# Optimization experiments

Measured on AMD Instinct MI355X. Metric: run time of the kernel, lower is better.

Reference implementation:

```python
import jax, jax.numpy as jnp
import numpy as np

M = 256      # num memories in bnn_history
D = 7686     # input_size (2 agent one-hot + 7680 embedding + 4 scalars)
H = 256      # NEAT hidden nodes
O = 4        # NEAT output nodes
N = D + H + O  # total nodes in dense weight matrix


def setup_inputs() -> dict:
    key = jax.random.key(0)
    ks = jax.random.split(key, 8)
    inv_sqrt_d = 1.0 / np.sqrt(D).astype(np.float32)
    return {
        "input_matrix": jax.random.normal(ks[0], (M, D), jnp.float32),
        "Wq": jax.random.normal(ks[1], (D, D), jnp.float32) * inv_sqrt_d,
        "bq": jnp.zeros((D,), jnp.float32),
        "Wk": jax.random.normal(ks[2], (D, D), jnp.float32) * inv_sqrt_d,
        "bk": jnp.zeros((D,), jnp.float32),
        "Wv": jax.random.normal(ks[3], (D, D), jnp.float32) * inv_sqrt_d,
        "bv": jnp.zeros((D,), jnp.float32),
        "weight_mu": jax.random.normal(ks[4], (N, N), jnp.float32) * 0.01,
        "weight_sigma": jnp.full((N, N), 0.1, jnp.float32),  # build_network inits sigma to 0.1
        "bias_mu": jnp.zeros((H + O,), jnp.float32),
        "bias_sigma": jnp.full((H + O,), 0.1, jnp.float32),
        "eps_w": jax.random.normal(ks[5], (N, N), jnp.float32),
        "eps_b": jax.random.normal(ks[6], (H + O,), jnp.float32),
    }


def reference(input_matrix, Wq, bq, Wk, bk, Wv, bv,
              weight_mu, weight_sigma, bias_mu, bias_sigma, eps_w, eps_b):
    # --- attention over memory rows (nn.Linear applies x @ W.T + b) ---
    Q = input_matrix @ Wq.T + bq            # [M, D]
    K = input_matrix @ Wk.T + bk            # [M, D]
    V = input_matrix @ Wv.T + bv            # [M, D]
    scale = 1.0 / jnp.sqrt(jnp.asarray(D, input_matrix.dtype))
    attn = jax.nn.softmax((Q @ K.T) * scale, axis=-1)  # [M, M]
    context = (attn @ V).mean(axis=0)       # [D] pooled attended context

    # --- Bayesian reparameterized genome weights / biases ---
    W = weight_mu + weight_sigma * eps_w    # [N, N], W[i, j] = weight of edge i->j
    b = bias_mu + bias_sigma * eps_b        # [H+O]

    # --- topological NEAT-style evaluation: inputs, then hidden, then outputs ---
    values0 = jnp.zeros((N,), input_matrix.dtype).at[:D].set(context)

    def step(values, j):
        col = jax.lax.dynamic_slice_in_dim(W, j, 1, axis=1)[:, 0]  # incoming weights of node j
        pre = values @ col + b[j - D]        # sum aggregation + bias
        return values.at[j].set(jnp.tanh(pre)), None

    values, _ = jax.lax.scan(step, values0, jnp.arange(D, N))
    return values[-O:]                       # output node activations
```

## Files before the change

kernel.cpp:

```cpp
#include <hip/hip_runtime.h>
#include <hip/hip_bf16.h>
#include <type_traits>

#define DIN   7686
#define NNODE 7946
#define HOUT  260
#define KP    8192
#define BROW  1036

typedef __attribute__((ext_vector_type(8))) short bf16x8;
typedef __attribute__((ext_vector_type(4))) float f32x4;
typedef __attribute__((ext_vector_type(2))) float f32x2;

__device__ __forceinline__ unsigned int f2b(float f) {
  union { float f; unsigned int u; } v; v.f = f;
  return (v.u + 0x7FFFu + ((v.u >> 16) & 1u)) >> 16;
}
__device__ __forceinline__ unsigned int pack2(float lo, float hi) {
  unsigned int r;
  asm("v_cvt_pk_bf16_f32 %0, %1, %2" : "=v"(r) : "v"(lo), "v"(hi));
  return r;
}
__device__ __forceinline__ float b2f(unsigned short h) {
  union { unsigned int u; float f; } v; v.u = ((unsigned int)h) << 16; return v.f;
}
__device__ __forceinline__ float readlane_f(float v, int lane) {
  return __uint_as_float(__builtin_amdgcn_readlane(__float_as_uint(v), lane));
}

__global__ void prep_x2(const float* __restrict__ X, char* __restrict__ XbT2)
{
  const int m = blockIdx.x, t = threadIdx.x;
  const float* row = X + (size_t)m * DIN;
  const int i16 = m >> 4;
#pragma unroll
  for (int c2 = 0; c2 < 4; ++c2) {
    const int k8 = (c2 * 256 + t) * 8;
    float f[8];
    if (k8 + 8 <= DIN) {
#pragma unroll
      for (int h = 0; h < 4; ++h) {
        float2 v = *(const float2*)(row + k8 + h * 2);
        f[h * 2] = v.x; f[h * 2 + 1] = v.y;
      }
    } else {
#pragma unroll
      for (int h = 0; h < 8; ++h) f[h] = (k8 + h < DIN) ? row[k8 + h] : 0.f;
    }
    uint4 o;
    o.x = pack2(f[0], f[1]); o.y = pack2(f[2], f[3]);
    o.z = pack2(f[4], f[5]); o.w = pack2(f[6], f[7]);
    const int kc = k8 >> 7, kk = k8 & 127, ks = kk >> 5, hq = (kk & 31) >> 3;
    const int lane = (m & 15) + (hq << 4);
    char* dst = XbT2 + ((((size_t)kc * 16 + i16) * 4 + ks) << 10) + lane * 16;
    *(uint4*)dst = o;
  }
}

__global__ __launch_bounds__(512, 4)
void gemm_qk9(const char* __restrict__ XbT2,
              const float* __restrict__ Wq, const float* __restrict__ Wk,
              const float* __restrict__ bq, const float* __restrict__ bk,
              unsigned short* __restrict__ Qbf, unsigned short* __restrict__ Kbf)
{
  const int nt = blockIdx.x, mat = blockIdx.y;
  const float* W = mat ? Wk : Wq;
  const float* bias = mat ? bk : bq;
  unsigned short* Out = mat ? Kbf : Qbf;
  const int n0 = nt * 32;
  const int tid = threadIdx.x, l = tid & 63, wv = tid >> 6;
  const int lm = l & 15, hq = l >> 4;

  __shared__ __align__(16) unsigned short Bp[32 * BROW];

  const long long DD = (long long)DIN * DIN;

  f32x4 acc[2][2] = {};
  bf16x8 A0[2], A1[2], A2[2];
  f32x4 F[16];

  long long rb[4];
#pragma unroll
  for (int r = 0; r < 4; ++r) {
    int grow = n0 + wv * 4 + r; if (grow > DIN - 1) grow = DIN - 1;
    rb[r] = (long long)grow * DIN;
  }

#define LOADW(z_) {                                                       \
    const int k0_ = (z_) * 1024;                                          \
    _Pragma("unroll")                                                     \
    for (int r_ = 0; r_ < 4; ++r_)                                        \
      _Pragma("unroll")                                                   \
      for (int c_ = 0; c_ < 4; ++c_) {                                    \
        long long gi_ = rb[r_] + k0_ + c_ * 256 + l * 4;                  \
        if (gi_ > DD - 4) gi_ = DD - 4;       \
        F[r_ * 4 + c_] = __builtin_nontemporal_load((const f32x4*)(W + gi_)); \
      } }

#define WRITEW() {                                                        \
    _Pragma("unroll")                                                     \
    for (int r_ = 0; r_ < 4; ++r_) {                                      \
      unsigned short* dr_ = &Bp[(wv * 4 + r_) * BROW];                    \
      _Pragma("unroll")                                                   \
      for (int c_ = 0; c_ < 4; ++c_) {                                    \
        f32x4 v_ = F[r_ * 4 + c_];                                        \
        uint2 o_; o_.x = pack2(v_[0], v_[1]); o_.y = pack2(v_[2], v_[3]); \
        *(uint2*)(dr_ + c_ * 256 + l * 4) = o_;                           \
      } } }

#define LA(dst, z_, s_) {                                                 \
    const int kc_ = (z_) * 8 + ((s_) >> 2), ks_ = (s_) & 3;               \
    const char* b_ = XbT2 +                                               \
        ((((size_t)kc_ * 16 + 2 * wv) * 4 + ks_) << 10) + l * 16;         \
    dst[0] = *(const bf16x8*)b_;                                          \
    dst[1] = *(const bf16x8*)(b_ + 4096); }

#define STEP(Ar, s_) {                                                    \
    bf16x8 b0_ = *(const bf16x8*)&Bp[lm * BROW + (s_) * 32 + hq * 8];     \
    bf16x8 b1_ = *(const bf16x8*)&Bp[(16 + lm) * BROW + (s_) * 32 + hq * 8]; \
    acc[0][0] = __builtin_amdgcn_mfma_f32_16x16x32_bf16(Ar[0], b0_, acc[0][0], 0, 0, 0); \
    acc[0][1] = __builtin_amdgcn_mfma_f32_16x16x32_bf16(Ar[0], b1_, acc[0][1], 0, 0, 0); \
    acc[1][0] = __builtin_amdgcn_mfma_f32_16x16x32_bf16(Ar[1], b0_, acc[1][0], 0, 0, 0); \
    acc[1][1] = __builtin_amdgcn_mfma_f32_16x16x32_bf16(Ar[1], b1_, acc[1][1], 0, 0, 0); }

#pragma unroll 1
  for (int z = 0; z < 8; ++z) {
    if (z) __syncthreads();

    LOADW(z)
    WRITEW()
    __syncthreads();

    LA(A0, z, 0) LA(A1, z, 1) LA(A2, z, 2)
#pragma unroll 1
    for (int su = 0; su < 30; su += 3) {
      STEP(A0, su + 0)
      if (su + 3 < 32) LA(A0, z, su + 3)
      STEP(A1, su + 1)
      if (su + 4 < 32) LA(A1, z, su + 4)
      STEP(A2, su + 2)
      if (su + 5 < 32) LA(A2, z, su + 5)
    }
    STEP(A0, 30)
    STEP(A1, 31)
  }
#undef LOADW
#undef WRITEW
#undef LA
#undef STEP

#pragma unroll
  for (int i = 0; i < 2; ++i) {
    const int r0 = (2 * wv + i) * 16 + hq * 4;
#pragma unroll
    for (int j = 0; j < 2; ++j) {
      const int col = n0 + j * 16 + lm;
      const float bb = (col < DIN) ? bias[col] : 0.f;
#pragma unroll
      for (int q = 0; q < 4; ++q) {
        const float v = acc[i][j][q] + bb;
        Out[(size_t)(r0 + q) * KP + col] = (col < DIN) ? (unsigned short)f2b(v) : 0;
      }
    }
  }
}

__global__ __launch_bounds__(512)
void gemm_logits(const unsigned short* __restrict__ Qbf,
                 const unsigned short* __restrict__ Kbf, float* __restrict__ LP)
{
  const int qr = blockIdx.x & 1, qc = blockIdx.x >> 1, z = blockIdx.z;
  const int tid = threadIdx.x, lane = tid & 63, wv = tid >> 6;
  const int lm = lane & 15, lq = (lane >> 4) * 8;
  const int rowBase = qr * 128 + (wv & 3) * 32;
  const int colBase = qc * 128 + (wv >> 2) * 64;
  const int k0 = z * 512;
  f32x4 acc[2][4] = {};
#pragma unroll 4
  for (int ks = 0; ks < 16; ++ks) {
    bf16x8 a[2], b[4];
#pragma unroll
    for (int i = 0; i < 2; ++i)
      a[i] = *(const bf16x8*)(Qbf + (size_t)(rowBase + i * 16 + lm) * KP + k0 + ks * 32 + lq);
#pragma unroll
    for (int j = 0; j < 4; ++j)
      b[j] = *(const bf16x8*)(Kbf + (size_t)(colBase + j * 16 + lm) * KP + k0 + ks * 32 + lq);
#pragma unroll
    for (int i = 0; i < 2; ++i)
#pragma unroll
      for (int j = 0; j < 4; ++j)
        acc[i][j] = __builtin_amdgcn_mfma_f32_16x16x32_bf16(a[i], b[j], acc[i][j], 0, 0, 0);
  }
  float* out = LP + (size_t)z * 65536;
#pragma unroll
  for (int i = 0; i < 2; ++i) {
    const int r0 = rowBase + i * 16 + (lane >> 4) * 4;
#pragma unroll
    for (int j = 0; j < 4; ++j) {
      const int col = colBase + j * 16 + lm;
#pragma unroll
      for (int q = 0; q < 4; ++q)
        out[(size_t)(r0 + q) * 256 + col] = acc[i][j][q];
    }
  }
}

__global__ void softmax_fused(const float* __restrict__ LP, float* __restrict__ abar)
{
  __shared__ float red[8];
  const int m = blockIdx.x, t = threadIdx.x;
  float v = 0.f;
#pragma unroll
  for (int zz = 0; zz < 16; ++zz) v += LP[(size_t)zz * 65536 + m * 256 + t];
  const float scale = 1.0f / sqrtf((float)DIN);
  float mx = v;
#pragma unroll
  for (int o = 32; o >= 1; o >>= 1) mx = fmaxf(mx, __shfl_xor(mx, o, 64));
  if ((t & 63) == 0) red[t >> 6] = mx;
  __syncthreads();
  mx = fmaxf(fmaxf(red[0], red[1]), fmaxf(red[2], red[3]));
  float e = __expf((v - mx) * scale);
  float s = e;
#pragma unroll
  for (int o = 32; o >= 1; o >>= 1) s += __shfl_xor(s, o, 64);
  if ((t & 63) == 0) red[4 + (t >> 6)] = s;
  __syncthreads();
  s = red[4] + red[5] + red[6] + red[7];
  atomicAdd(&abar[t], e * (1.0f / 256.0f) / s);
}

__global__ void y_kernel(const float* __restrict__ X, const float* __restrict__ abar,
                         float* __restrict__ y)
{
  __shared__ float ab[256];
  ab[threadIdx.x] = abar[threadIdx.x];
  __syncthreads();
  const int c = blockIdx.x * 256 + threadIdx.x;
  if (c >= DIN) return;
  float s = 0.f;
#pragma unroll 8
  for (int m = 0; m < 256; ++m) s += ab[m] * X[(size_t)m * DIN + c];
  y[c] = s;
}

__global__ __launch_bounds__(512)
void ctx_mv(const float* __restrict__ Wv, const float* __restrict__ y,
            const float* __restrict__ bv, float* __restrict__ ctx)
{
  const int wv = threadIdx.x >> 6, l = threadIdx.x & 63;
  const int row = blockIdx.x * 8 + wv;
  if (row >= DIN) return;
  const float* wr_ = Wv + (size_t)row * DIN;
  float s = 0.f;
#pragma unroll 5
  for (int it = 0; it < 30; ++it) {
    const int k = it * 256 + l * 4;
    f32x4 w4 = __builtin_nontemporal_load((const f32x4*)(wr_ + k));
    float4 y4 = *(const float4*)(y + k);
    s = fmaf(w4[0], y4.x, s);
    s = fmaf(w4[1], y4.y, s);
    s = fmaf(w4[2], y4.z, s);
    s = fmaf(w4[3], y4.w, s);
  }
  if (l < 6) s += wr_[7680 + l] * y[7680 + l];
#pragma unroll
  for (int o = 32; o >= 1; o >>= 1) s += __shfl_xor(s, o, 64);
  if (l == 0) ctx[row] = s + bv[row];
}

__global__ void base_kernel(const float* __restrict__ mu, const float* __restrict__ sg,
                            const float* __restrict__ ep, const float* __restrict__ ctx,
                            float* __restrict__ base)
{
  const int j = threadIdx.x;
  if (j >= HOUT) return;
  const int i0 = blockIdx.x * 31;
  const int i1 = min(i0 + 31, DIN);
  float acc = 0.f;
#pragma unroll 4
  for (int i = i0; i < i1; ++i) {
    const size_t idx = (size_t)i * NNODE + DIN + j;
    acc = fmaf(ctx[i], fmaf(sg[idx], ep[idx], mu[idx]), acc);
  }
  atomicAdd(&base[j], acc);
}

__global__ void ws_kernel(const float* __restrict__ mu, const float* __restrict__ sg,
                          const float* __restrict__ ep, float* __restrict__ WsG)
{
  const int t = blockIdx.x;
  const int j = threadIdx.x;
  if (j >= HOUT) return;
  const size_t idx = (size_t)(DIN + t) * NNODE + DIN + j;
  WsG[t * HOUT + j] = fmaf(sg[idx], ep[idx], mu[idx]);
}

__global__ __launch_bounds__(64, 1)
void scan2(const float* __restrict__ WsG, const float* __restrict__ base,
           const float* __restrict__ bmu, const float* __restrict__ bsg,
           const float* __restrict__ epb, float* __restrict__ out)
{
  __shared__ __align__(16) float tile[32 * HOUT + 128];
  const int l = threadIdx.x;

  float a0, a1, a2, a3, a4;
  {
    int j = l;       a0 = base[j] + bmu[j] + bsg[j] * epb[j];
    j = l + 64;      a1 = base[j] + bmu[j] + bsg[j] * epb[j];
    j = l + 128;     a2 = base[j] + bmu[j] + bsg[j] * epb[j];
    j = l + 192;     a3 = base[j] + bmu[j] + bsg[j] * epb[j];
    j = l + 256;     a4 = (j < HOUT) ? (base[j] + bmu[j] + bsg[j] * epb[j]) : 0.f;
  }

  float4 stg[33];
  auto LOADT = [&](int tb) {
    const int nfl = ((tb == 8) ? 4 : 32) * HOUT;
    const float* src = WsG + tb * 32 * HOUT;
#pragma unroll
    for (int c = 0; c < 33; ++c) {
      const int o = c * 256 + l * 4;
      if (o < nfl) stg[c] = *(const float4*)(src + o);
    }
  };
  auto WRITET = [&](int tb) {
    const int nfl = ((tb == 8) ? 4 : 32) * HOUT;
#pragma unroll
    for (int c = 0; c < 33; ++c) {
      const int o = c * 256 + l * 4;
      if (o < nfl) *(float4*)&tile[o] = stg[c];
    }
  };

  float w0, w1, w2, w3, w4;
  auto PRER = [&](int trow) {
    const float* tr = tile + trow * HOUT;
    w0 = tr[l]; w1 = tr[l + 64]; w2 = tr[l + 128]; w3 = tr[l + 192]; w4 = tr[l + 256];
  };

  auto inner = [&](auto Bc, int tb, int nrows) {
    constexpr int B = Bc.value;
    for (int tt = 0; tt < nrows; ++tt) {
      const int t = tb * 32 + tt;
      float pre;
      if constexpr (B == 0) pre = readlane_f(a0, t & 63);
      else if constexpr (B == 1) pre = readlane_f(a1, t & 63);
      else if constexpr (B == 2) pre = readlane_f(a2, t & 63);
      else if constexpr (B == 3) pre = readlane_f(a3, t & 63);
      else pre = readlane_f(a4, t & 63);
      const float pc = fminf(fmaxf(pre, -12.f), 12.f);
      const float e = __expf(2.f * pc);
      const float vt = 1.f - 2.f / (e + 1.f);
      if (t >= 256 && l == 0) out[t - 256] = vt;
      if (l > t)            a0 = fmaf(vt, w0, a0);
      if (l + 64 > t)       a1 = fmaf(vt, w1, a1);
      if (l + 128 > t)      a2 = fmaf(vt, w2, a2);
      if (l + 192 > t)      a3 = fmaf(vt, w3, a3);
      if (l + 256 > t && l + 256 < HOUT) a4 = fmaf(vt, w4, a4);
      if (tt + 1 < nrows) PRER(tt + 1);
    }
  };

  LOADT(0); WRITET(0); PRER(0);

#define TILE_STEP(tb, B, nr)                                    \
  { if ((tb) < 8) LOADT((tb) + 1);                              \
    inner(std::integral_constant<int, B>{}, (tb), (nr));        \
    if ((tb) < 8) { WRITET((tb) + 1); PRER(0); } }

  TILE_STEP(0, 0, 32)
  TILE_STEP(1, 0, 32)
  TILE_STEP(2, 1, 32)
  TILE_STEP(3, 1, 32)
  TILE_STEP(4, 2, 32)
  TILE_STEP(5, 2, 32)
  TILE_STEP(6, 3, 32)
  TILE_STEP(7, 3, 32)
  TILE_STEP(8, 4, 4)
#undef TILE_STEP
}

extern "C" void kernel_launch(void* const* d_in, const int* in_sizes, int n_in,
                              void* d_out, int out_size, void* d_ws, size_t ws_size,
                              hipStream_t stream)
{
  const float* X   = (const float*)d_in[0];
  const float* Wq  = (const float*)d_in[1];
  const float* bq  = (const float*)d_in[2];
  const float* Wk  = (const float*)d_in[3];
  const float* bk  = (const float*)d_in[4];
  const float* Wv  = (const float*)d_in[5];
  const float* bv  = (const float*)d_in[6];
  const float* wmu = (const float*)d_in[7];
  const float* wsg = (const float*)d_in[8];
  const float* bmu = (const float*)d_in[9];
  const float* bsg = (const float*)d_in[10];
  const float* epw = (const float*)d_in[11];
  const float* epb = (const float*)d_in[12];

  char* p = (char*)d_ws;
  auto alloc = [&](size_t bytes) -> char* {
    char* r = p;
    p += (bytes + 255) & ~(size_t)255;
    return r;
  };
  char* XbT2 = alloc((size_t)64 * 65536);
  unsigned short* Qbf = (unsigned short*)alloc((size_t)256 * KP * 2);
  unsigned short* Kbf = (unsigned short*)alloc((size_t)256 * KP * 2);
  float* LP   = (float*)alloc((size_t)16 * 65536 * 4);
  float* abar = (float*)alloc(256 * 4);
  float* y    = (float*)alloc(7686 * 4);
  float* ctx  = (float*)alloc(7686 * 4);
  float* base = (float*)alloc(HOUT * 4);
  float* WsG  = (float*)alloc((size_t)HOUT * HOUT * 4 + 1024);

  prep_x2<<<dim3(256), dim3(256), 0, stream>>>(X, XbT2);
  (void)hipMemsetAsync(abar, 0, 256 * 4, stream);
  (void)hipMemsetAsync(base, 0, HOUT * 4, stream);
  (void)hipMemsetAsync(Qbf, 0, (size_t)256 * KP * 2, stream);
  (void)hipMemsetAsync(Kbf, 0, (size_t)256 * KP * 2, stream);

  gemm_qk9<<<dim3(241, 2), dim3(512), 0, stream>>>(XbT2, Wq, Wk, bq, bk, Qbf, Kbf);
  gemm_logits<<<dim3(4, 1, 16), dim3(512), 0, stream>>>(Qbf, Kbf, LP);
  softmax_fused<<<dim3(256), dim3(256), 0, stream>>>(LP, abar);
  y_kernel<<<dim3(31), dim3(256), 0, stream>>>(X, abar, y);
  ctx_mv<<<dim3(961), dim3(512), 0, stream>>>(Wv, y, bv, ctx);
  base_kernel<<<dim3(256), dim3(320), 0, stream>>>(wmu, wsg, epw, ctx, base);
  ws_kernel<<<dim3(260), dim3(320), 0, stream>>>(wmu, wsg, epw, WsG);
  scan2<<<dim3(1), dim3(64), 0, stream>>>(WsG, base, bmu, bsg, epb, (float*)d_out);
}
```

Before: 350.1 us.

## Widen QK GEMM tile to 64 columns with smaller K chunks; move ws_kernel earlier

The Q/K projection kernel now computes 64 output columns per block instead of 32, with K staged in chunks of 512 instead of 1024. The chunk is loaded in two register halves to cap register use. Each A fragment loaded from global memory now feeds 8 MFMAs instead of 4, halving the re-reads of the activation matrix across blocks. The grid shrinks from 241 to 121 blocks per matrix, which reduces parallelism, and there are twice as many sync rounds. The independent ws_kernel launch is also moved earlier in the stream.

```diff
diff --git a/kernel.cpp b/kernel.cpp
--- a/kernel.cpp
+++ b/kernel.cpp
@@ -6,7 +6,7 @@
 #define NNODE 7946
 #define HOUT  260
 #define KP    8192
-#define BROW  1036
+#define PROW  520
 
 typedef __attribute__((ext_vector_type(8))) short bf16x8;
 typedef __attribute__((ext_vector_type(4))) float f32x4;
@@ -58,94 +58,92 @@
 }
 
 __global__ __launch_bounds__(512, 4)
-void gemm_qk9(const char* __restrict__ XbT2,
-              const float* __restrict__ Wq, const float* __restrict__ Wk,
-              const float* __restrict__ bq, const float* __restrict__ bk,
-              unsigned short* __restrict__ Qbf, unsigned short* __restrict__ Kbf)
+void gemm_qk10(const char* __restrict__ XbT2,
+               const float* __restrict__ Wq, const float* __restrict__ Wk,
+               const float* __restrict__ bq, const float* __restrict__ bk,
+               unsigned short* __restrict__ Qbf, unsigned short* __restrict__ Kbf)
 {
   const int nt = blockIdx.x, mat = blockIdx.y;
   const float* W = mat ? Wk : Wq;
   const float* bias = mat ? bk : bq;
   unsigned short* Out = mat ? Kbf : Qbf;
-  const int n0 = nt * 32;
+  const int n0 = nt * 64;
   const int tid = threadIdx.x, l = tid & 63, wv = tid >> 6;
   const int lm = l & 15, hq = l >> 4;
 
-  __shared__ __align__(16) unsigned short Bp[32 * BROW];
+  __shared__ __align__(16) unsigned short Bp[64 * PROW];
 
   const long long DD = (long long)DIN * DIN;
 
-  f32x4 acc[2][2] = {};
-  bf16x8 A0[2], A1[2], A2[2];
-  f32x4 F[16];
-
-  long long rb[4];
-#pragma unroll
-  for (int r = 0; r < 4; ++r) {
-    int grow = n0 + wv * 4 + r; if (grow > DIN - 1) grow = DIN - 1;
-    rb[r] = (long long)grow * DIN;
-  }
-
-#define LOADW(z_) {                                                       \
-    const int k0_ = (z_) * 1024;                                          \
-    _Pragma("unroll")                                                     \
-    for (int r_ = 0; r_ < 4; ++r_)                                        \
-      _Pragma("unroll")                                                   \
-      for (int c_ = 0; c_ < 4; ++c_) {                                    \
-        long long gi_ = rb[r_] + k0_ + c_ * 256 + l * 4;                  \
-        if (gi_ > DD - 4) gi_ = DD - 4;       \
-        F[r_ * 4 + c_] = __builtin_nontemporal_load((const f32x4*)(W + gi_)); \
-      } }
-
-#define WRITEW() {                                                        \
+  f32x4 acc[2][4] = {};
+  bf16x8 A0[2], A1[2];
+  f32x4 F[8];
+
+#define LOADH(z_, rh_) {                                                  \
     _Pragma("unroll")                                                     \
     for (int r_ = 0; r_ < 4; ++r_) {                                      \
-      unsigned short* dr_ = &Bp[(wv * 4 + r_) * BROW];                    \
+      int grow_ = n0 + wv * 8 + (rh_) * 4 + r_;                           \
+      if (grow_ > DIN - 1) grow_ = DIN - 1;                               \
+      const long long gb_ = (long long)grow_ * DIN + (z_) * 512;          \
       _Pragma("unroll")                                                   \
-      for (int c_ = 0; c_ < 4; ++c_) {                                    \
-        f32x4 v_ = F[r_ * 4 + c_];                                        \
+      for (int c_ = 0; c_ < 2; ++c_) {                                    \
+        long long gi_ = gb_ + c_ * 256 + l * 4;                           \
+        if (gi_ > DD - 4) gi_ = DD - 4;       \
+        F[r_ * 2 + c_] = __builtin_nontemporal_load((const f32x4*)(W + gi_)); \
+      } } }
+
+#define WRITEH(rh_) {                                                     \
+    _Pragma("unroll")                                                     \
+    for (int r_ = 0; r_ < 4; ++r_) {                                      \
+      unsigned short* dr_ = &Bp[(wv * 8 + (rh_) * 4 + r_) * PROW];        \
+      _Pragma("unroll")                                                   \
+      for (int c_ = 0; c_ < 2; ++c_) {                                    \
+        f32x4 v_ = F[r_ * 2 + c_];                                        \
         uint2 o_; o_.x = pack2(v_[0], v_[1]); o_.y = pack2(v_[2], v_[3]); \
         *(uint2*)(dr_ + c_ * 256 + l * 4) = o_;                           \
       } } }
 
 #define LA(dst, z_, s_) {                                                 \
-    const int kc_ = (z_) * 8 + ((s_) >> 2), ks_ = (s_) & 3;               \
+    const int kc_ = (z_) * 4 + ((s_) >> 2), ks_ = (s_) & 3;               \
     const char* b_ = XbT2 +                                               \
         ((((size_t)kc_ * 16 + 2 * wv) * 4 + ks_) << 10) + l * 16;         \
     dst[0] = *(const bf16x8*)b_;                                          \
     dst[1] = *(const bf16x8*)(b_ + 4096); }
 
 #define STEP(Ar, s_) {                                                    \
-    bf16x8 b0_ = *(const bf16x8*)&Bp[lm * BROW + (s_) * 32 + hq * 8];     \
-    bf16x8 b1_ = *(const bf16x8*)&Bp[(16 + lm) * BROW + (s_) * 32 + hq * 8]; \
-    acc[0][0] = __builtin_amdgcn_mfma_f32_16x16x32_bf16(Ar[0], b0_, acc[0][0], 0, 0, 0); \
-    acc[0][1] = __builtin_amdgcn_mfma_f32_16x16x32_bf16(Ar[0], b1_, acc[0][1], 0, 0, 0); \
-    acc[1][0] = __builtin_amdgcn_mfma_f32_16x16x32_bf16(Ar[1], b0_, acc[1][0], 0, 0, 0); \
-    acc[1][1] = __builtin_amdgcn_mfma_f32_16x16x32_bf16(Ar[1], b1_, acc[1][1], 0, 0, 0); }
+    bf16x8 bf_[4];                                                        \
+    _Pragma("unroll")                                                     \
+    for (int j_ = 0; j_ < 4; ++j_)                                        \
+      bf_[j_] = *(const bf16x8*)&Bp[(j_ * 16 + lm) * PROW + (s_) * 32 + hq * 8]; \
+    _Pragma("unroll")                                                     \
+    for (int i_ = 0; i_ < 2; ++i_)                                        \
+      _Pragma("unroll")                                                   \
+      for (int j_ = 0; j_ < 4; ++j_)                                      \
+        acc[i_][j_] = __builtin_amdgcn_mfma_f32_16x16x32_bf16(Ar[i_], bf_[j_], acc[i_][j_], 0, 0, 0); }
 
 #pragma unroll 1
-  for (int z = 0; z < 8; ++z) {
+  for (int z = 0; z < 16; ++z) {
     if (z) __syncthreads();
 
-    LOADW(z)
-    WRITEW()
+    LOADH(z, 0)
+    WRITEH(0)
+    LOADH(z, 1)
+    WRITEH(1)
     __syncthreads();
 
-    LA(A0, z, 0) LA(A1, z, 1) LA(A2, z, 2)
+    LA(A0, z, 0) LA(A1, z, 1)
 #pragma unroll 1
-    for (int su = 0; su < 30; su += 3) {
+    for (int su = 0; su < 14; su += 2) {
       STEP(A0, su + 0)
-      if (su + 3 < 32) LA(A0, z, su + 3)
+      LA(A0, z, su + 2)
       STEP(A1, su + 1)
-      if (su + 4 < 32) LA(A1, z, su + 4)
-      STEP(A2, su + 2)
-      if (su + 5 < 32) LA(A2, z, su + 5)
-    }
-    STEP(A0, 30)
-    STEP(A1, 31)
-  }
-#undef LOADW
-#undef WRITEW
+      LA(A1, z, su + 3)
+    }
+    STEP(A0, 14)
+    STEP(A1, 15)
+  }
+#undef LOADH
+#undef WRITEH
 #undef LA
 #undef STEP
 
@@ -153,7 +151,7 @@
   for (int i = 0; i < 2; ++i) {
     const int r0 = (2 * wv + i) * 16 + hq * 4;
 #pragma unroll
-    for (int j = 0; j < 2; ++j) {
+    for (int j = 0; j < 4; ++j) {
       const int col = n0 + j * 16 + lm;
       const float bb = (col < DIN) ? bias[col] : 0.f;
 #pragma unroll
@@ -414,17 +412,17 @@
   float* WsG  = (float*)alloc((size_t)HOUT * HOUT * 4 + 1024);
 
   prep_x2<<<dim3(256), dim3(256), 0, stream>>>(X, XbT2);
+  ws_kernel<<<dim3(260), dim3(320), 0, stream>>>(wmu, wsg, epw, WsG);
   (void)hipMemsetAsync(abar, 0, 256 * 4, stream);
   (void)hipMemsetAsync(base, 0, HOUT * 4, stream);
   (void)hipMemsetAsync(Qbf, 0, (size_t)256 * KP * 2, stream);
   (void)hipMemsetAsync(Kbf, 0, (size_t)256 * KP * 2, stream);
 
-  gemm_qk9<<<dim3(241, 2), dim3(512), 0, stream>>>(XbT2, Wq, Wk, bq, bk, Qbf, Kbf);
+  gemm_qk10<<<dim3(121, 2), dim3(512), 0, stream>>>(XbT2, Wq, Wk, bq, bk, Qbf, Kbf);
   gemm_logits<<<dim3(4, 1, 16), dim3(512), 0, stream>>>(Qbf, Kbf, LP);
   softmax_fused<<<dim3(256), dim3(256), 0, stream>>>(LP, abar);
   y_kernel<<<dim3(31), dim3(256), 0, stream>>>(X, abar, y);
   ctx_mv<<<dim3(961), dim3(512), 0, stream>>>(Wv, y, bv, ctx);
   base_kernel<<<dim3(256), dim3(320), 0, stream>>>(wmu, wsg, epw, ctx, base);
-  ws_kernel<<<dim3(260), dim3(320), 0, stream>>>(wmu, wsg, epw, WsG);
   scan2<<<dim3(1), dim3(64), 0, stream>>>(WsG, base, bmu, bsg, epb, (float*)d_out);
 }
```

Measured after the change: 349.0 us. About the same (-0.3%).
